# Kernel optimization log

Measured on AMD Instinct MI355X. Metric: run time of the kernel, lower is better.

## Reference

```python
import jax, jax.numpy as jnp
import numpy as np
import math

N_HEAD = 8


def _rope(x):
    # x: [B, H, S, D]; lucidrains rotary_embedding_torch default: interleaved pairs, theta=10000
    D = x.shape[-1]
    S = x.shape[-2]
    inv_freq = 1.0 / (10000.0 ** (jnp.arange(0, D, 2, dtype=jnp.float32) / D))  # [D/2]
    t = jnp.arange(S, dtype=jnp.float32)
    freqs = jnp.repeat(t[:, None] * inv_freq[None, :], 2, axis=-1)  # [S, D] interleaved repeat
    cos = jnp.cos(freqs).astype(x.dtype)
    sin = jnp.sin(freqs).astype(x.dtype)
    xp = x.reshape(*x.shape[:-1], D // 2, 2)
    rot = jnp.stack((-xp[..., 1], xp[..., 0]), axis=-1).reshape(x.shape)  # rotate_half (interleaved)
    return x * cos + rot * sin


def _row_linear(x, Wo):
    # faithful RowLinear: transpose then flat-reshape back (a real permutation), linear, inverse shuffle
    B, S, P = x.shape
    E = Wo.shape[0]
    x = jnp.swapaxes(x, 1, 2).reshape(B, S, P)
    x = jnp.einsum('bsp,ep->bse', x, Wo)  # [B, S, E]
    x = x.reshape(B, E, -1)  # [B, E, S]
    return jnp.swapaxes(x, 1, 2)  # [B, S, E]


def setup_inputs() -> dict:
    key = jax.random.key(0)
    k0, k1, k2, k3, k4 = jax.random.split(key, 5)
    B, S, E, P = 4, 2048, 1024, 1024
    std = 1.0 / math.sqrt(E)
    return {
        'emb': jax.random.normal(k0, (B, S, E), dtype=jnp.float32),
        'W1': jax.random.normal(k1, (P, E), dtype=jnp.float32) * std,
        'W2': jax.random.normal(k2, (P, E), dtype=jnp.float32) * std,
        'W3': jax.random.normal(k3, (P, E), dtype=jnp.float32) * std,
        'Wo': jax.random.normal(k4, (E, P), dtype=jnp.float32) * std,
    }


def reference(emb, W1, W2, W3, Wo):
    B, S, E = emb.shape
    P = W1.shape[0]
    H = N_HEAD
    D = P // H
    q = jnp.einsum('bse,pe->bsp', emb, W1).reshape(B, H, S, D)  # raw view split (as in source)
    k = jnp.einsum('bse,pe->bsp', emb, W2).reshape(B, H, S, D)
    v = jnp.einsum('bse,pe->bsp', emb, W3).reshape(B, H, S, D)
    q = _rope(q)
    k = _rope(k)
    scores = jnp.einsum('bhqd,bhkd->bhqk', q, k).astype(jnp.float32) / math.sqrt(H)
    attn = jax.nn.softmax(scores, axis=-1).astype(v.dtype)
    out = jnp.einsum('bhqk,bhkd->bhqd', attn, v)  # [B, H, S, D]
    out = jnp.swapaxes(out, 1, 2).reshape(B, S, P)
    return _row_linear(out, Wo)
```

## Files before the change

kernel.cpp:

```cpp
#include <hip/hip_runtime.h>

typedef float f32x4 __attribute__((ext_vector_type(4)));
typedef float f32x16 __attribute__((ext_vector_type(16)));
typedef __bf16 bf16x8 __attribute__((ext_vector_type(8)));

__device__ __forceinline__ unsigned short f2bf(float f) {
  unsigned int u = __float_as_uint(f);
  u = (u + 0x7FFFu + ((u >> 16) & 1u)) >> 16;
  return (unsigned short)u;
}
__device__ __forceinline__ float bf2f(unsigned short u) {
  return __uint_as_float((unsigned int)u << 16);
}

__device__ __forceinline__ f32x4 mfma16(bf16x8 a, bf16x8 b, f32x4 c) {
  return __builtin_amdgcn_mfma_f32_16x16x32_bf16(a, b, c, 0, 0, 0);
}
__device__ __forceinline__ f32x16 mfma32(bf16x8 a, bf16x8 b, f32x16 c) {
  return __builtin_amdgcn_mfma_f32_32x32x16_bf16(a, b, c, 0, 0, 0);
}

__device__ __forceinline__ unsigned int cvtpk_bf16(float a, float b) {
  unsigned int r;
  asm("v_cvt_pk_bf16_f32 %0, %1, %2" : "=v"(r) : "v"(a), "v"(b));
  return r;
}
__device__ __forceinline__ void pl32swap(unsigned int& a, unsigned int& b) {
  asm("v_permlane32_swap_b32 %0, %1" : "+v"(a), "+v"(b));
}

__device__ __forceinline__ void load8_bf16(const unsigned short* p, unsigned short* d) {
  *(uint4*)d = *(const uint4*)p;
}
__device__ __forceinline__ void load8_bf16(const float* p, unsigned short* d) {
  float4 a = *(const float4*)p;
  float4 b = *(const float4*)(p + 4);
  __align__(16) unsigned short t[8] = {f2bf(a.x), f2bf(a.y), f2bf(a.z), f2bf(a.w),
                                       f2bf(b.x), f2bf(b.y), f2bf(b.z), f2bf(b.w)};
  *(uint4*)d = *(uint4*)t;
}

__device__ __forceinline__ void gload_lds16(const unsigned short* g, unsigned short* l) {
  __builtin_amdgcn_global_load_lds(
      (const __attribute__((address_space(1))) void*)g,
      (__attribute__((address_space(3))) void*)l, 16, 0, 0);
}

__device__ __forceinline__ void drain_barrier() {
  asm volatile("s_waitcnt vmcnt(0)" ::: "memory");
  __builtin_amdgcn_sched_barrier(0);
  __builtin_amdgcn_s_barrier();
  __builtin_amdgcn_sched_barrier(0);
}

__device__ __forceinline__ void wait2_barrier() {
  asm volatile("s_waitcnt vmcnt(2)" ::: "memory");
  __builtin_amdgcn_sched_barrier(0);
  __builtin_amdgcn_s_barrier();
  __builtin_amdgcn_sched_barrier(0);
}

__global__ __launch_bounds__(256) void convert_gen(const float* __restrict__ src,
                                                   unsigned short* __restrict__ dst) {
  int idx = (blockIdx.x * 256 + threadIdx.x) * 8;
  __align__(16) unsigned short t[8];
  load8_bf16(src + idx, t);
  *(uint4*)(dst + idx) = *(uint4*)t;
}

__global__ __launch_bounds__(256) void convert_w3(const float* __restrict__ W1,
                                                  const float* __restrict__ W2,
                                                  const float* __restrict__ W3,
                                                  unsigned short* __restrict__ dst) {
  int i = blockIdx.x;
  int sel = i >> 9;
  const float* src = (sel == 0) ? W1 : (sel == 1) ? W2 : W3;
  int w = i & 511;
  int t = threadIdx.x;
  int p = 2 * w + (t >> 7);
  int kc = t & 127;
  __align__(16) unsigned short tmp[8];
  load8_bf16(src + (size_t)p * 1024 + kc * 8, tmp);
  int lane = (kc & 3) * 16 + (p & 15);
  size_t idx16 = ((((size_t)(p >> 7) * 32 + (kc >> 2)) * 2 + ((p >> 6) & 1)) * 4 +
                  ((p >> 4) & 3)) * 64 + lane;
  *(uint4*)(dst + (size_t)sel * 1048576 + idx16 * 8) = *(uint4*)tmp;
}

__global__ __launch_bounds__(256) void convert_wo(const float* __restrict__ Wo,
                                                  unsigned short* __restrict__ dst) {
  int w = blockIdx.x;
  int t = threadIdx.x;
  int p = 2 * w + (t >> 7);
  int kc = t & 127;
  __align__(16) unsigned short tmp[8];
  load8_bf16(Wo + (size_t)p * 1024 + kc * 8, tmp);
  int lane = (kc & 3) * 16 + (p & 15);
  size_t idx16 = ((((size_t)(p >> 7) * 32 + (kc >> 2)) * 2 + ((p >> 6) & 1)) * 4 +
                  ((p >> 4) & 3)) * 64 + lane;
  *(uint4*)(dst + idx16 * 8) = *(uint4*)tmp;
}

__global__ __launch_bounds__(256) void gemm_qkv(const unsigned short* __restrict__ A,
                                                const unsigned short* __restrict__ WBf,
                                                unsigned short* __restrict__ q,
                                                unsigned short* __restrict__ k,
                                                unsigned short* __restrict__ v) {
  __shared__ __align__(16) unsigned short As[3][128][32];
  const int t = threadIdx.x;
  const int lane = t & 63;
  const int wid = t >> 6;
  const int quad = lane >> 4;
  const int l16 = lane & 15;
  const int wm = (wid >> 1) << 6;
  const int wn = (wid & 1) << 6;
  const int sel = blockIdx.x >> 3;
  const int nb = blockIdx.x & 7;
  const int mbase = blockIdx.y * 128;
  unsigned short* C = (sel == 0) ? q : (sel == 1) ? k : v;

  const unsigned short* aSrc0 = A + (size_t)(mbase + (t >> 2)) * 1024 + ((t & 3) << 3);
  const unsigned short* aSrc1 = A + (size_t)(mbase + 64 + (t >> 2)) * 1024 + ((t & 3) << 3);
  unsigned short* aDst0 = &As[0][0][0] + t * 8;
  unsigned short* aDst1 = &As[0][0][0] + 2048 + t * 8;
  auto stageA = [&](int k0, int p) {
    gload_lds16(aSrc0 + k0, aDst0 + p * 4096);
    gload_lds16(aSrc1 + k0, aDst1 + p * 4096);
  };

  const unsigned short* pB = WBf + (size_t)sel * 1048576 +
                             ((size_t)(nb * 64 + (wid & 1)) * 4) * 512 + lane * 8;

  f32x4 acc[4][4] = {};

  stageA(0, 0);
  stageA(32, 1);
  asm volatile("s_waitcnt vmcnt(2)" ::: "memory");
  __builtin_amdgcn_sched_barrier(0);
  __builtin_amdgcn_s_barrier();
  __builtin_amdgcn_sched_barrier(0);

  int p = 0;
  for (int k0 = 0; k0 < 1024; k0 += 32) {
    bf16x8 bfr[4];
#pragma unroll
    for (int nt = 0; nt < 4; ++nt) bfr[nt] = *(const bf16x8*)(pB + nt * 512);
    pB += 4096;
    if (k0 + 64 < 1024) stageA(k0 + 64, p == 0 ? 2 : p - 1);
    bf16x8 af[4];
#pragma unroll
    for (int mt = 0; mt < 4; ++mt)
      af[mt] = *(const bf16x8*)(&As[p][wm + mt * 16 + l16][quad * 8]);
#pragma unroll
    for (int nt = 0; nt < 4; ++nt)
#pragma unroll
      for (int mt = 0; mt < 4; ++mt)
        acc[mt][nt] = mfma16(af[mt], bfr[nt], acc[mt][nt]);
    wait2_barrier();
    p = (p == 2) ? 0 : p + 1;
  }

  const bool rope = (sel < 2);
#pragma unroll
  for (int mt = 0; mt < 4; ++mt) {
#pragma unroll
    for (int nt = 0; nt < 4; ++nt) {
#pragma unroll
      for (int r = 0; r < 4; ++r) {
        int row_g = mbase + wm + mt * 16 + quad * 4 + r;
        int col_g = (nb << 7) + wn + nt * 16 + l16;
        float val = acc[mt][nt][r];
        if (rope) {
          float other = __shfl_xor(val, 1);
          int s = (((row_g & 2047) << 3) + (col_g >> 7)) & 2047;
          int d = col_g & 127;
          float invf = __expf(-0.14391156f * (float)(d >> 1));
          float ang = (float)s * invf;
          float sv, cv;
          __sincosf(ang, &sv, &cv);
          val = (d & 1) ? (val * cv + other * sv) : (val * cv - other * sv);
        }
        C[(size_t)row_g * 1024 + col_g] = f2bf(val);
      }
    }
  }
}

__global__ __launch_bounds__(256) void transpose_v(const unsigned short* __restrict__ Vn,
                                                   unsigned short* __restrict__ VT) {
  __shared__ __align__(16) unsigned short tile[64][72];
  const int t = threadIdx.x;
  const int s0 = blockIdx.x * 64;
  const int d0 = blockIdx.y * 64;
  const int bh = blockIdx.z;
  const size_t base = (size_t)bh * (2048 * 128);
#pragma unroll
  for (int i = 0; i < 2; ++i) {
    int c = t + (i << 8);
    int sr = c >> 3;
    int dc = (c & 7) << 3;
    *(uint4*)(&tile[sr][dc]) = *(const uint4*)(Vn + base + (size_t)(s0 + sr) * 128 + d0 + dc);
  }
  __syncthreads();
#pragma unroll
  for (int i = 0; i < 2; ++i) {
    int c = t + (i << 8);
    int dr = c >> 3;
    int sc = (c & 7) << 3;
    __align__(16) unsigned short tmp[8];
#pragma unroll
    for (int j = 0; j < 8; ++j) tmp[j] = tile[sc + j][dr];
    *(uint4*)(VT + base + (size_t)(d0 + dr) * 2048 + s0 + sc) = *(uint4*)tmp;
  }
}

__global__ __launch_bounds__(256) void gemm_out(const unsigned short* __restrict__ OT,
                                                const unsigned short* __restrict__ Bf,
                                                float* __restrict__ C) {
  __shared__ __align__(16) char smem_raw[34816];
  const int t = threadIdx.x;
  const int lane = t & 63;
  const int wid = t >> 6;
  const int quad = lane >> 4;
  const int l16 = lane & 15;
  const int wm = (wid >> 1) << 6;
  const int wn = (wid & 1) << 6;
  const int mbase = blockIdx.y * 128;
  const int nbx = blockIdx.x;

  const unsigned short* aSrcs[2];
#pragma unroll
  for (int i = 0; i < 2; ++i) {
    int c = t + (i << 8);
    int row = c >> 2;
    int col = (c & 3) << 3;
    int R = mbase + row;
    int b = R >> 11;
    int ii = R & 2047;
    aSrcs[i] = OT + (size_t)(b * 8 + (ii >> 8)) * (128 * 2048) +
               (size_t)((ii >> 1) & 127) * 2048 + ((ii & 1) << 10) + col;
  }
  unsigned short* smE = (unsigned short*)smem_raw;
  auto stageA = [&](int k0, int p) {
    gload_lds16(aSrcs[0] + k0, smE + p * 4096 + t * 8);
    gload_lds16(aSrcs[1] + k0, smE + p * 4096 + 2048 + t * 8);
  };

  const unsigned short* pB = Bf + ((size_t)(nbx * 64 + (wid & 1)) * 4) * 512 + lane * 8;

  f32x4 acc[4][4] = {};

  stageA(0, 0);
  stageA(32, 1);
  asm volatile("s_waitcnt vmcnt(2)" ::: "memory");
  __builtin_amdgcn_sched_barrier(0);
  __builtin_amdgcn_s_barrier();
  __builtin_amdgcn_sched_barrier(0);

  int p = 0;
  for (int k0 = 0; k0 < 1024; k0 += 32) {
    bf16x8 bfr[4];
#pragma unroll
    for (int nt = 0; nt < 4; ++nt) bfr[nt] = *(const bf16x8*)(pB + nt * 512);
    pB += 4096;
    if (k0 + 64 < 1024) stageA(k0 + 64, p == 0 ? 2 : p - 1);
    auto As = (unsigned short(*)[32])(smem_raw + p * 8192);
    bf16x8 af[4];
#pragma unroll
    for (int mt = 0; mt < 4; ++mt)
      af[mt] = *(const bf16x8*)(&As[wm + mt * 16 + l16][quad * 8]);
#pragma unroll
    for (int nt = 0; nt < 4; ++nt)
#pragma unroll
      for (int mt = 0; mt < 4; ++mt)
        acc[mt][nt] = mfma16(af[mt], bfr[nt], acc[mt][nt]);
    wait2_barrier();
    p = (p == 2) ? 0 : p + 1;
  }

  float(*Ts)[68] = (float(*)[68])smem_raw;
  const int b = mbase >> 11;
  const int ebase = (mbase & 2047) >> 1;
#pragma unroll
  for (int p2 = 0; p2 < 2; ++p2) {
    __syncthreads();
#pragma unroll
    for (int mt = 0; mt < 4; ++mt)
#pragma unroll
      for (int nt = 0; nt < 4; ++nt)
#pragma unroll
        for (int rr = p2; rr < 4; rr += 2) {
          int col_local = wn + nt * 16 + l16;
          int row_local = wm + mt * 16 + quad * 4 + rr;
          Ts[col_local][row_local >> 1] = acc[mt][nt][rr];
        }
    __syncthreads();
    int srow = t >> 1;
    int e0 = (t & 1) << 5;
    float* dst = C + (size_t)b * 2097152 +
                 (size_t)(p2 * 1024 + nbx * 128 + srow) * 1024 + ebase + e0;
#pragma unroll
    for (int j = 0; j < 8; ++j)
      ((float4*)dst)[j] = *(const float4*)&Ts[srow][e0 + j * 4];
  }
}

__global__ __launch_bounds__(256, 2) void flash_attn(const unsigned short* __restrict__ Q,
                                                     const unsigned short* __restrict__ Kg,
                                                     const unsigned short* __restrict__ VTg,
                                                     unsigned short* __restrict__ OT) {
  __shared__ __align__(16) char sm[65536];
  const int t = threadIdx.x;
  const int lane = t & 63;
  const int wid = t >> 6;
  const int l31 = lane & 31;
  const int hi = lane >> 5;
  const int x16 = (l31 & 7) << 4;
  const int i = blockIdx.x;
  const int bh = (i & 7) + ((i >> 3) & 3) * 8;
  const int qbase = (i >> 5) << 7;
  const size_t base = (size_t)bh * (2048 * 128);
  const float sl2 = 0.51006976f;

  const unsigned short* Kg_b = Kg + base;
  const unsigned short* Vg_b = VTg + base;

  auto issueKV = [&](int kvoff, int pbit) {
    unsigned short* Kl = (unsigned short*)(sm + (pbit << 14));
    unsigned short* Vl = (unsigned short*)(sm + 32768 + (pbit << 14));
#pragma unroll
    for (int j = 0; j < 4; ++j) {
      int c = t + (j << 8);
      int row = c >> 4, ch = c & 15;
      gload_lds16(Kg_b + (size_t)(kvoff + row) * 128 + ((ch ^ (row & 7)) << 3),
                  Kl + c * 8);
      int d = c >> 3, cv = c & 7;
      gload_lds16(Vg_b + (size_t)d * 2048 + kvoff + ((cv ^ (d & 7)) << 3), Vl + c * 8);
    }
  };

  bf16x8 qf[8];
  {
    const unsigned short* qp = Q + base + (size_t)(qbase + wid * 32 + l31) * 128 + hi * 8;
#pragma unroll
    for (int ks = 0; ks < 8; ++ks) qf[ks] = *(const bf16x8*)(qp + ks * 16);
  }

  f32x16 accO[4] = {};
  float l = 0.f;

  issueKV(0, 0);
  drain_barrier();

  for (int kv = 0; kv < 2048; kv += 64) {
    const int p = (kv >> 6) & 1;
    if (kv + 64 < 2048) issueKV(kv + 64, p ^ 1);
    const char* Kb = sm + (p << 14);
    const char* Vb = sm + 32768 + (p << 14);

    f32x16 s0 = {}, s1 = {};
#pragma unroll
    for (int ks = 0; ks < 8; ++ks) {
      int cb = (ks * 32 + hi * 16) ^ x16;
      bf16x8 k0 = *(const bf16x8*)(Kb + l31 * 256 + cb);
      bf16x8 k1 = *(const bf16x8*)(Kb + 8192 + l31 * 256 + cb);
      s0 = mfma32(k0, qf[ks], s0);
      s1 = mfma32(k1, qf[ks], s1);
    }

#pragma unroll
    for (int r = 0; r < 16; ++r) s0[r] = exp2f(s0[r] * sl2);
#pragma unroll
    for (int r = 0; r < 16; ++r) s1[r] = exp2f(s1[r] * sl2);
    float t8[8];
#pragma unroll
    for (int r = 0; r < 8; ++r)
      t8[r] = (s0[r] + s0[r + 8]) + (s1[r] + s1[r + 8]);
#pragma unroll
    for (int d = 4; d > 0; d >>= 1)
#pragma unroll
      for (int r = 0; r < d; ++r) t8[r] += t8[r + d];
    l += t8[0] + __shfl_xor(t8[0], 32);

    bf16x8 pfrag[4];
#pragma unroll
    for (int kb = 0; kb < 4; ++kb) {
      const f32x16& S = (kb < 2) ? s0 : s1;
      const int b = (kb & 1) * 8;
      unsigned int a0 = cvtpk_bf16(S[b + 0], S[b + 1]);
      unsigned int a1 = cvtpk_bf16(S[b + 2], S[b + 3]);
      unsigned int a2 = cvtpk_bf16(S[b + 4], S[b + 5]);
      unsigned int a3 = cvtpk_bf16(S[b + 6], S[b + 7]);
      pl32swap(a0, a2);
      pl32swap(a1, a3);
      union { unsigned int u[4]; bf16x8 v; } pu;
      pu.u[0] = a0; pu.u[1] = a1; pu.u[2] = a2; pu.u[3] = a3;
      pfrag[kb] = pu.v;
    }

#pragma unroll
    for (int dt = 0; dt < 4; ++dt) {
#pragma unroll
      for (int kb = 0; kb < 4; ++kb) {
        bf16x8 vfr = *(const bf16x8*)(Vb + l31 * 128 + dt * 4096 +
                                      ((kb * 32 + hi * 16) ^ x16));
        accO[dt] = mfma32(vfr, pfrag[kb], accO[dt]);
      }
    }

    drain_barrier();
  }

  auto To = (unsigned short(*)[136])sm;
  const float invl = 1.f / l;
  const int qloc = wid * 32 + l31;
#pragma unroll
  for (int dt = 0; dt < 4; ++dt)
#pragma unroll
    for (int r = 0; r < 16; ++r) {
      int d = dt * 32 + (r & 3) + ((r >> 2) << 3) + hi * 4;
      To[d][qloc] = f2bf(accO[dt][r] * invl);
    }
  __syncthreads();
  int dr = t >> 1;
  int off = (t & 1) << 6;
  unsigned short* dst = OT + base + (size_t)dr * 2048 + qbase + off;
#pragma unroll
  for (int j = 0; j < 8; ++j)
    ((uint4*)dst)[j] = *(const uint4*)&To[dr][off + j * 8];
}

extern "C" void kernel_launch(void* const* d_in, const int* in_sizes, int n_in,
                              void* d_out, int out_size, void* d_ws, size_t ws_size,
                              hipStream_t stream) {
  const float* emb = (const float*)d_in[0];
  const float* W1  = (const float*)d_in[1];
  const float* W2  = (const float*)d_in[2];
  const float* W3  = (const float*)d_in[3];
  const float* Wo  = (const float*)d_in[4];
  float* out = (float*)d_out;

  const size_t NELEM = (size_t)8 * 1024 * 1024;
  unsigned short* q     = (unsigned short*)d_ws;
  unsigned short* k     = q + NELEM;
  unsigned short* vn    = k + NELEM;
  unsigned short* X     = vn + NELEM;
  unsigned short* oT    = vn;
  unsigned short* vT    = X;
  unsigned short* W123B = X;
  unsigned short* WoB   = X;
  unsigned short* embB  = (unsigned short*)d_out;

  dim3 blk(256, 1, 1);
  convert_w3<<<dim3(1536), blk, 0, stream>>>(W1, W2, W3, W123B);
  convert_gen<<<dim3(4096), blk, 0, stream>>>(emb, embB);
  gemm_qkv<<<dim3(24, 64), blk, 0, stream>>>(embB, W123B, q, k, vn);
  transpose_v<<<dim3(32, 2, 32), blk, 0, stream>>>(vn, vT);
  flash_attn<<<dim3(512, 1, 1), blk, 0, stream>>>(q, k, vT, oT);
  convert_wo<<<dim3(512), blk, 0, stream>>>(Wo, WoB);
  gemm_out<<<dim3(8, 64), blk, 0, stream>>>(oT, WoB, out);
}
```

Measured before the change: 317.2 us.

## Compute Q, K and V in one GEMM block to share the A tile

The QKV projection kernel now has each block compute all three outputs (Q, K, V) for its 128x128 tile, so each A tile loaded into LDS is reused three times instead of being loaded once per projection. The grid shrinks from 24x64 to 8x64 blocks. The LDS pipeline drops from triple to double buffering with a full drain barrier each iteration, and launch bounds request 2 blocks per CU. The tradeoffs are three times the accumulator registers (48 f32x4), fewer blocks to fill the GPU, and less overlap between loads and compute.

```diff
diff --git a/kernel.cpp b/kernel.cpp
--- a/kernel.cpp
+++ b/kernel.cpp
@@ -101,12 +101,12 @@
   *(uint4*)(dst + idx16 * 8) = *(uint4*)tmp;
 }
 
-__global__ __launch_bounds__(256) void gemm_qkv(const unsigned short* __restrict__ A,
-                                                const unsigned short* __restrict__ WBf,
-                                                unsigned short* __restrict__ q,
-                                                unsigned short* __restrict__ k,
-                                                unsigned short* __restrict__ v) {
-  __shared__ __align__(16) unsigned short As[3][128][32];
+__global__ __launch_bounds__(256, 2) void gemm_qkv(const unsigned short* __restrict__ A,
+                                                   const unsigned short* __restrict__ WBf,
+                                                   unsigned short* __restrict__ q,
+                                                   unsigned short* __restrict__ k,
+                                                   unsigned short* __restrict__ v) {
+  __shared__ __align__(16) unsigned short As[2][128][32];
   const int t = threadIdx.x;
   const int lane = t & 63;
   const int wid = t >> 6;
@@ -114,10 +114,8 @@
   const int l16 = lane & 15;
   const int wm = (wid >> 1) << 6;
   const int wn = (wid & 1) << 6;
-  const int sel = blockIdx.x >> 3;
-  const int nb = blockIdx.x & 7;
+  const int nb = blockIdx.x;
   const int mbase = blockIdx.y * 128;
-  unsigned short* C = (sel == 0) ? q : (sel == 1) ? k : v;
 
   const unsigned short* aSrc0 = A + (size_t)(mbase + (t >> 2)) * 1024 + ((t & 3) << 3);
   const unsigned short* aSrc1 = A + (size_t)(mbase + 64 + (t >> 2)) * 1024 + ((t & 3) << 3);
@@ -128,59 +126,62 @@
     gload_lds16(aSrc1 + k0, aDst1 + p * 4096);
   };
 
-  const unsigned short* pB = WBf + (size_t)sel * 1048576 +
-                             ((size_t)(nb * 64 + (wid & 1)) * 4) * 512 + lane * 8;
-
-  f32x4 acc[4][4] = {};
+  const unsigned short* pB = WBf + (size_t)nb * 131072 + (wid & 1) * 2048 + lane * 8;
+
+  f32x4 acc[3][4][4] = {};
 
   stageA(0, 0);
-  stageA(32, 1);
-  asm volatile("s_waitcnt vmcnt(2)" ::: "memory");
-  __builtin_amdgcn_sched_barrier(0);
-  __builtin_amdgcn_s_barrier();
-  __builtin_amdgcn_sched_barrier(0);
+  drain_barrier();
 
   int p = 0;
   for (int k0 = 0; k0 < 1024; k0 += 32) {
-    bf16x8 bfr[4];
-#pragma unroll
-    for (int nt = 0; nt < 4; ++nt) bfr[nt] = *(const bf16x8*)(pB + nt * 512);
-    pB += 4096;
-    if (k0 + 64 < 1024) stageA(k0 + 64, p == 0 ? 2 : p - 1);
+    if (k0 + 32 < 1024) stageA(k0 + 32, p ^ 1);
     bf16x8 af[4];
 #pragma unroll
     for (int mt = 0; mt < 4; ++mt)
       af[mt] = *(const bf16x8*)(&As[p][wm + mt * 16 + l16][quad * 8]);
 #pragma unroll
-    for (int nt = 0; nt < 4; ++nt)
-#pragma unroll
-      for (int mt = 0; mt < 4; ++mt)
-        acc[mt][nt] = mfma16(af[mt], bfr[nt], acc[mt][nt]);
-    wait2_barrier();
-    p = (p == 2) ? 0 : p + 1;
-  }
-
-  const bool rope = (sel < 2);
-#pragma unroll
-  for (int mt = 0; mt < 4; ++mt) {
-#pragma unroll
-    for (int nt = 0; nt < 4; ++nt) {
-#pragma unroll
-      for (int r = 0; r < 4; ++r) {
-        int row_g = mbase + wm + mt * 16 + quad * 4 + r;
-        int col_g = (nb << 7) + wn + nt * 16 + l16;
-        float val = acc[mt][nt][r];
-        if (rope) {
-          float other = __shfl_xor(val, 1);
-          int s = (((row_g & 2047) << 3) + (col_g >> 7)) & 2047;
-          int d = col_g & 127;
-          float invf = __expf(-0.14391156f * (float)(d >> 1));
-          float ang = (float)s * invf;
-          float sv, cv;
-          __sincosf(ang, &sv, &cv);
-          val = (d & 1) ? (val * cv + other * sv) : (val * cv - other * sv);
+    for (int sel = 0; sel < 3; ++sel) {
+      bf16x8 bfr[4];
+#pragma unroll
+      for (int nt = 0; nt < 4; ++nt)
+        bfr[nt] = *(const bf16x8*)(pB + (size_t)sel * 1048576 + nt * 512);
+#pragma unroll
+      for (int nt = 0; nt < 4; ++nt)
+#pragma unroll
+        for (int mt = 0; mt < 4; ++mt)
+          acc[sel][mt][nt] = mfma16(af[mt], bfr[nt], acc[sel][mt][nt]);
+    }
+    pB += 4096;
+    drain_barrier();
+    p ^= 1;
+  }
+
+#pragma unroll
+  for (int sel = 0; sel < 3; ++sel) {
+    unsigned short* C = (sel == 0) ? q : (sel == 1) ? k : v;
+    const bool rope = (sel < 2);
+#pragma unroll
+    for (int mt = 0; mt < 4; ++mt) {
+#pragma unroll
+      for (int nt = 0; nt < 4; ++nt) {
+#pragma unroll
+        for (int r = 0; r < 4; ++r) {
+          int row_g = mbase + wm + mt * 16 + quad * 4 + r;
+          int col_g = (nb << 7) + wn + nt * 16 + l16;
+          float val = acc[sel][mt][nt][r];
+          if (rope) {
+            float other = __shfl_xor(val, 1);
+            int s = (((row_g & 2047) << 3) + (col_g >> 7)) & 2047;
+            int d = col_g & 127;
+            float invf = __expf(-0.14391156f * (float)(d >> 1));
+            float ang = (float)s * invf;
+            float sv, cv;
+            __sincosf(ang, &sv, &cv);
+            val = (d & 1) ? (val * cv + other * sv) : (val * cv - other * sv);
+          }
+          C[(size_t)row_g * 1024 + col_g] = f2bf(val);
         }
-        C[(size_t)row_g * 1024 + col_g] = f2bf(val);
       }
     }
   }
@@ -454,7 +455,7 @@
   dim3 blk(256, 1, 1);
   convert_w3<<<dim3(1536), blk, 0, stream>>>(W1, W2, W3, W123B);
   convert_gen<<<dim3(4096), blk, 0, stream>>>(emb, embB);
-  gemm_qkv<<<dim3(24, 64), blk, 0, stream>>>(embB, W123B, q, k, vn);
+  gemm_qkv<<<dim3(8, 64), blk, 0, stream>>>(embB, W123B, q, k, vn);
   transpose_v<<<dim3(32, 2, 32), blk, 0, stream>>>(vn, vT);
   flash_attn<<<dim3(512, 1, 1), blk, 0, stream>>>(q, k, vT, oT);
   convert_wo<<<dim3(512), blk, 0, stream>>>(Wo, WoB);
```

After: 332.6 us. 4.9% more time.
